# Performance work log

Measured on AMD Instinct MI355X. Metric: run time of the kernel, lower is better.

The kernel has to match this reference:

```python
import jax, jax.numpy as jnp
import numpy as np

B, T, DIM, H, DH, DT = 2, 2048, 1024, 16, 64, 32
Q_TEMP, K_TEMP = 1.0, 1.0
EPS = float(np.finfo(np.float32).eps)  # torch RMSNorm default eps for fp32
INV_SQRT_DH = 1.0 / np.sqrt(DH)


def _get_time(length, head_time_delta, time_angles, with_time_delta):
    # [T,1,1] positions, optionally offset per head -> [T,H,1]
    pos = jnp.arange(length, dtype=jnp.float32)[:, None, None]
    if with_time_delta:
        pos = pos + head_time_delta[None, :, None]          # [T,H,1]
    else:
        pos = jnp.broadcast_to(pos, (length, H, 1))          # [T,H,1]
    ang = pos * time_angles                                  # [T,H,Dt]
    c, s = jnp.cos(ang), jnp.sin(ang)
    return jnp.concatenate([c + s, c - s], axis=-1) * INV_SQRT_DH  # [T,H,2Dt]


def setup_inputs() -> dict:
    key = jax.random.key(0)
    ks = jax.random.split(key, 6)
    sc = 0.02
    states = jax.random.normal(ks[0], (B, T, DIM), jnp.float32)
    attention_mask = jnp.ones((B, T), jnp.int32)
    ln_w = jnp.ones((DIM,), jnp.float32)
    time_angles = 10000.0 ** (-1.0 / jnp.arange(1, DT + 1, dtype=jnp.float32))
    head_time_delta = jax.random.uniform(ks[1], (H,), jnp.float32)
    Wq = jax.random.normal(ks[2], (H * DH, DIM), jnp.float32) * sc
    q_bias = jnp.zeros((H * DH,), jnp.float32)
    Wk = jax.random.normal(ks[3], (H * DH, DIM), jnp.float32) * sc
    bk = jnp.zeros((H * DH,), jnp.float32)
    Wv = jax.random.normal(ks[4], (H * DH, DIM), jnp.float32) * sc
    bv = jnp.zeros((H * DH,), jnp.float32)
    Wo = jax.random.normal(ks[5], (DIM, H * DH), jnp.float32) * sc
    bo = jnp.zeros((DIM,), jnp.float32)
    return dict(states=states, attention_mask=attention_mask, ln_w=ln_w,
                time_angles=time_angles, head_time_delta=head_time_delta,
                Wq=Wq, q_bias=q_bias, Wk=Wk, bk=bk, Wv=Wv, bv=bv, Wo=Wo, bo=bo)


def reference(states, attention_mask, ln_w, time_angles, head_time_delta,
              Wq, q_bias, Wk, bk, Wv, bv, Wo, bo):
    # RMSNorm
    x = states * jax.lax.rsqrt(jnp.mean(states * states, axis=-1, keepdims=True) + EPS) * ln_w
    m = attention_mask.astype(x.dtype)[:, :, None, None]   # [B,T,1,1]

    # Q path -> q_attentioned [B,T,T,H]
    q = (x @ Wq.T - jnp.exp(q_bias)).reshape(B, T, H, DH)
    q_sm = jax.nn.softmax(q / Q_TEMP * m, axis=-1)
    t_q = _get_time(T, head_time_delta, time_angles, True)   # [T,H,2Dt]
    t_k = _get_time(T, head_time_delta, time_angles, False)  # [T,H,2Dt]
    q_timed = jnp.sum(q_sm, axis=-1, keepdims=True) * t_q    # [B,T,H,2Dt]
    q_att = jnp.einsum('bthd,lhd->btlh', q_timed, t_k)       # [B,T,T,H]

    # KV path
    k = (x @ Wk.T + bk).reshape(B, T, H, DH)
    k_sm = jax.nn.softmax(k / K_TEMP * m, axis=-1)
    v = (x @ Wv.T + bv).reshape(B, T, H, DH)
    kv = k_sm * v                                            # [B,T,H,Dh]

    loading = jnp.einsum('btlh,blhd->bthd', q_att, kv)       # [B,T,H,Dh]
    return loading.reshape(B, T, DIM) @ Wo.T + bo
```

## Files before the change

kernel.cpp:

```cpp
#include <hip/hip_runtime.h>
#include <math.h>

#define T_ 2048
#define H_ 16

typedef __attribute__((ext_vector_type(8))) short bfx8;
typedef __attribute__((ext_vector_type(4))) float f32x4;

__device__ __forceinline__ short f2bf(float f) {
  union { float f; unsigned u; } x; x.f = f;
  unsigned r = (x.u + 0x7FFFu + ((x.u >> 16) & 1u)) >> 16;
  return (short)r;
}
__device__ __forceinline__ float bf2f(short s) {
  union { unsigned u; float f; } x;
  x.u = ((unsigned)(unsigned short)s) << 16;
  return x.f;
}

#define GLD_LDS(g, l) \
  __builtin_amdgcn_global_load_lds( \
      (const __attribute__((address_space(1))) void*)(g), \
      (__attribute__((address_space(3))) void*)(l), 16, 0, 0)

__global__ __launch_bounds__(256) void prep_kernel(
    const float* __restrict__ Wk, const float* __restrict__ Wv,
    const float* __restrict__ Wo, const float* __restrict__ angles,
    const float* __restrict__ states, const float* __restrict__ ln_w,
    short* __restrict__ Wkb, short* __restrict__ Wvb, short* __restrict__ Wob,
    short* __restrict__ xb, short* __restrict__ Cb, short* __restrict__ tkT,
    float* __restrict__ MtH) {
  const int blk = blockIdx.x;
  if (blk < 3072) {
    const int i = blk * 256 + threadIdx.x;
    const int which = i >> 18;
    const int idx = i & 262143;
    const float* s = (which == 0) ? Wk : (which == 1) ? Wv : Wo;
    short* d = (which == 0) ? Wkb : (which == 1) ? Wvb : Wob;
    const float4 v = ((const float4*)s)[idx];
    short4 r;
    r.x = f2bf(v.x); r.y = f2bf(v.y); r.z = f2bf(v.z); r.w = f2bf(v.w);
    ((short4*)d)[idx] = r;
  } else if (blk < 7168) {
    const int row = blk - 3072;
    const int tid = threadIdx.x;
    const float4 v = ((const float4*)(states + (size_t)row * 1024))[tid];
    float ss = v.x * v.x + v.y * v.y + v.z * v.z + v.w * v.w;
#pragma unroll
    for (int off = 32; off >= 1; off >>= 1) ss += __shfl_xor(ss, off);
    __shared__ float red[4];
    if ((tid & 63) == 0) red[tid >> 6] = ss;
    __syncthreads();
    const float tot = red[0] + red[1] + red[2] + red[3];
    const float scale = rsqrtf(tot * (1.0f / 1024.0f) + 1.1920928955078125e-07f);
    const float4 w = ((const float4*)ln_w)[tid];
    short4 o;
    o.x = f2bf(v.x * scale * w.x);
    o.y = f2bf(v.y * scale * w.y);
    o.z = f2bf(v.z * scale * w.z);
    o.w = f2bf(v.w * scale * w.w);
    ((short4*)(xb + (size_t)row * 1024))[tid] = o;
  } else if (blk < 7424) {
    const int gid = (blk - 7168) * 256 + threadIdx.x;
    const int j = gid & 31;
    const int t = gid >> 5;
    float s, c;
    sincosf((float)t * angles[j], &s, &c);
    Cb[(size_t)t * 64 + j] = f2bf(0.125f * c);
    Cb[(size_t)t * 64 + 32 + j] = f2bf(0.125f * s);
  } else if (blk < 7456) {
    const int gid = (blk - 7424) * 256 + threadIdx.x;
    const int tc = gid & 255;
    const int j = gid >> 8;
    const float th = angles[j];
    short lo[8], hi[8];
#pragma unroll
    for (int r = 0; r < 8; ++r) {
      float s, c;
      sincosf((float)(tc * 8 + r) * th, &s, &c);
      lo[r] = f2bf((c + s) * 0.125f);
      hi[r] = f2bf((c - s) * 0.125f);
    }
    short* base = tkT + (size_t)j * 2048 + tc * 8;
    *(short4*)(base) = *(short4*)&lo[0];
    *(short4*)(base + 4) = *(short4*)&lo[4];
    short* base2 = tkT + (size_t)(32 + j) * 2048 + tc * 8;
    *(short4*)(base2) = *(short4*)&hi[0];
    *(short4*)(base2 + 4) = *(short4*)&hi[4];
  } else {
    const int gid = (blk - 7456) * 256 + threadIdx.x;
    ((float4*)MtH)[gid] = make_float4(0.f, 0.f, 0.f, 0.f);
  }
}

__global__ __launch_bounds__(256) void kvgemm_kernel(
    const short* __restrict__ xb, const short* __restrict__ Wkb,
    const short* __restrict__ Wvb, const float* __restrict__ bk,
    const float* __restrict__ bv, const int* __restrict__ mask,
    const short* __restrict__ tkT, float* __restrict__ Mt) {
  __shared__ short smem[16384];
  __shared__ short Vs[128][64];
  short(*As)[64] = (short(*)[64])smem;
  short(*Bk)[64] = (short(*)[64])(smem + 8192);
  short(*Bv)[64] = (short(*)[64])(smem + 12288);
  short(*kvS)[132] = (short(*)[132])smem;

  const int row0 = blockIdx.x * 128;
  const int h = blockIdx.y;
  const int t = threadIdx.x;
  const int lane = t & 63;
  const int wv = t >> 6;
  const bool isV = wv >= 2;
  const int wrow = (wv & 1) * 64;
  const int lrow = lane & 15;

  const int srow8 = t >> 3;
  const int kslotS = (t & 7) ^ (srow8 & 7);
  const short* gaS = xb + (size_t)(row0 + srow8) * 1024 + kslotS * 8;
  const short* gkS = Wkb + (size_t)(h * 64 + srow8) * 1024 + kslotS * 8;
  const short* gvS = Wvb + (size_t)(h * 64 + srow8) * 1024 + kslotS * 8;
  short* laS = &As[srow8][(t & 7) * 8];
  short* lkS = &Bk[srow8][(t & 7) * 8];
  short* lvS = &Bv[srow8][(t & 7) * 8];

  f32x4 acc[4][4] = {};
  for (int k0 = 0; k0 < 1024; k0 += 64) {
    GLD_LDS(gaS + k0, laS);
    GLD_LDS(gaS + 32 * 1024 + k0, laS + 2048);
    GLD_LDS(gaS + 64 * 1024 + k0, laS + 4096);
    GLD_LDS(gaS + 96 * 1024 + k0, laS + 6144);
    GLD_LDS(gkS + k0, lkS);
    GLD_LDS(gkS + 32 * 1024 + k0, lkS + 2048);
    GLD_LDS(gvS + k0, lvS);
    GLD_LDS(gvS + 32 * 1024 + k0, lvS + 2048);
    __syncthreads();
#pragma unroll
    for (int kk = 0; kk < 2; ++kk) {
      const int pcol = ((kk * 4 + (lane >> 4)) ^ (lrow & 7)) * 8;
      bfx8 af[4], bf_[4];
#pragma unroll
      for (int i = 0; i < 4; ++i)
        af[i] = *(const bfx8*)&As[wrow + i * 16 + lrow][pcol];
      const short(*Bs)[64] = isV ? Bv : Bk;
#pragma unroll
      for (int j = 0; j < 4; ++j)
        bf_[j] = *(const bfx8*)&Bs[j * 16 + lrow][pcol];
#pragma unroll
      for (int i = 0; i < 4; ++i)
#pragma unroll
        for (int j = 0; j < 4; ++j)
          acc[i][j] = __builtin_amdgcn_mfma_f32_16x16x32_bf16(af[i], bf_[j], acc[i][j], 0, 0, 0);
    }
    __syncthreads();
  }
  const int rq = (lane >> 4) * 4;
  if (isV) {
#pragma unroll
    for (int j = 0; j < 4; ++j) {
      const float bb = bv[h * 64 + j * 16 + lrow];
#pragma unroll
      for (int i = 0; i < 4; ++i)
#pragma unroll
        for (int rr = 0; rr < 4; ++rr)
          Vs[wrow + rq + i * 16 + rr][j * 16 + lrow] = f2bf(acc[i][j][rr] + bb);
    }
  }
  __syncthreads();
  if (!isV) {
    float bkc[4];
#pragma unroll
    for (int j = 0; j < 4; ++j) bkc[j] = bk[h * 64 + j * 16 + lrow];
    const int rowg0 = row0 + wrow + rq;
#pragma unroll
    for (int i = 0; i < 4; ++i) {
#pragma unroll
      for (int rr = 0; rr < 4; ++rr) {
        const float m = (float)mask[rowg0 + i * 16 + rr];
        float kf[4];
#pragma unroll
        for (int j = 0; j < 4; ++j) kf[j] = (acc[i][j][rr] + bkc[j]) * m;
        float mx = fmaxf(fmaxf(kf[0], kf[1]), fmaxf(kf[2], kf[3]));
#pragma unroll
        for (int off = 8; off >= 1; off >>= 1) mx = fmaxf(mx, __shfl_xor(mx, off));
        float s = 0.0f;
#pragma unroll
        for (int j = 0; j < 4; ++j) { kf[j] = expf(kf[j] - mx); s += kf[j]; }
#pragma unroll
        for (int off = 8; off >= 1; off >>= 1) s += __shfl_xor(s, off);
        const float inv = 1.0f / s;
#pragma unroll
        for (int j = 0; j < 4; ++j)
          acc[i][j][rr] = kf[j] * inv *
                          bf2f(Vs[wrow + rq + i * 16 + rr][j * 16 + lrow]);
      }
    }
#pragma unroll
    for (int j = 0; j < 4; ++j) {
      const int d = j * 16 + lrow;
#pragma unroll
      for (int i = 0; i < 4; ++i) {
        short4 o;
        o.x = f2bf(acc[i][j][0]); o.y = f2bf(acc[i][j][1]);
        o.z = f2bf(acc[i][j][2]); o.w = f2bf(acc[i][j][3]);
        *(short4*)&kvS[d][wrow + rq + i * 16] = o;
      }
    }
  }
  __syncthreads();
  const int bb = row0 >> 11;
  const int tb = row0 & 2047;
  const short* tkb = tkT + (size_t)(wv * 16 + lrow) * 2048 + tb;
  const int kg = (lane >> 4) * 8;
  f32x4 macc[4] = {};
#pragma unroll
  for (int kc = 0; kc < 4; ++kc) {
    const bfx8 af = *(const bfx8*)(tkb + kc * 32 + kg);
#pragma unroll
    for (int j = 0; j < 4; ++j) {
      const bfx8 bf_ = *(const bfx8*)&kvS[j * 16 + lrow][kc * 32 + kg];
      macc[j] = __builtin_amdgcn_mfma_f32_16x16x32_bf16(af, bf_, macc[j], 0, 0, 0);
    }
  }
  float* Mb = Mt + (size_t)(bb * 16 + h) * 4096;
#pragma unroll
  for (int j = 0; j < 4; ++j) {
    const int d = j * 16 + lrow;
#pragma unroll
    for (int rr = 0; rr < 4; ++rr) {
      const int e = wv * 16 + rq + rr;
      atomicAdd(&Mb[(size_t)e * 64 + d], macc[j][rr]);
    }
  }
}

__global__ __launch_bounds__(256) void foldhgemm_kernel(
    const short* __restrict__ Wob, const float* __restrict__ Mt,
    const float* __restrict__ angles, const float* __restrict__ delta,
    float* __restrict__ H) {
  const int bid = blockIdx.x;
  const int t = threadIdx.x;
  const int lane = t & 63;
  const int w = t >> 6;
  const int lrow = lane & 15;
  const int kg = (lane >> 4) * 8;
  const int h2 = bid & 7;
  const int ot = (bid >> 3) & 15;
  const int b = bid >> 7;
  const int orow = ot * 64 + w * 16 + lrow;
  float p[2][2], q[2][2];
#pragma unroll
  for (int hh = 0; hh < 2; ++hh) {
    const float dl = delta[h2 * 2 + hh];
#pragma unroll
    for (int aa = 0; aa < 2; ++aa) {
      float s, c;
      sincosf(dl * angles[aa * 16 + lrow], &s, &c);
      p[hh][aa] = c + s;
      q[hh][aa] = c - s;
    }
  }
  f32x4 acc[4] = {};
#pragma unroll
  for (int ks = 0; ks < 4; ++ks) {
    const int hh = ks >> 1;
    const int h = h2 * 2 + hh;
    const int d0 = (ks & 1) * 32 + kg;
    const float* Mthb = Mt + (size_t)(b * 16 + h) * 4096;
    const bfx8 af = *(const bfx8*)(Wob + (size_t)orow * 1024 + h * 64 + d0);
    float m0a[8], m1a[8], m0b[8], m1b[8];
    *(float4*)&m0a[0] = *(const float4*)(Mthb + lrow * 64 + d0);
    *(float4*)&m0a[4] = *(const float4*)(Mthb + lrow * 64 + d0 + 4);
    *(float4*)&m1a[0] = *(const float4*)(Mthb + (32 + lrow) * 64 + d0);
    *(float4*)&m1a[4] = *(const float4*)(Mthb + (32 + lrow) * 64 + d0 + 4);
    *(float4*)&m0b[0] = *(const float4*)(Mthb + (16 + lrow) * 64 + d0);
    *(float4*)&m0b[4] = *(const float4*)(Mthb + (16 + lrow) * 64 + d0 + 4);
    *(float4*)&m1b[0] = *(const float4*)(Mthb + (48 + lrow) * 64 + d0);
    *(float4*)&m1b[4] = *(const float4*)(Mthb + (48 + lrow) * 64 + d0 + 4);
    bfx8 bf0, bf1, bf2, bf3;
#pragma unroll
    for (int e = 0; e < 8; ++e) {
      bf0[e] = f2bf(p[hh][0] * m0a[e] + q[hh][0] * m1a[e]);
      bf1[e] = f2bf(p[hh][1] * m0b[e] + q[hh][1] * m1b[e]);
      bf2[e] = f2bf(q[hh][0] * m0a[e] - p[hh][0] * m1a[e]);
      bf3[e] = f2bf(q[hh][1] * m0b[e] - p[hh][1] * m1b[e]);
    }
    acc[0] = __builtin_amdgcn_mfma_f32_16x16x32_bf16(af, bf0, acc[0], 0, 0, 0);
    acc[1] = __builtin_amdgcn_mfma_f32_16x16x32_bf16(af, bf1, acc[1], 0, 0, 0);
    acc[2] = __builtin_amdgcn_mfma_f32_16x16x32_bf16(af, bf2, acc[2], 0, 0, 0);
    acc[3] = __builtin_amdgcn_mfma_f32_16x16x32_bf16(af, bf3, acc[3], 0, 0, 0);
  }
  float* Hb = H + (size_t)b * 65536;
  const int rq = (lane >> 4) * 4;
#pragma unroll
  for (int j = 0; j < 4; ++j) {
    const int kap = j * 16 + lrow;
#pragma unroll
    for (int rr = 0; rr < 4; ++rr) {
      const int o = ot * 64 + w * 16 + rq + rr;
      atomicAdd(&Hb[(size_t)o * 64 + kap], acc[j][rr]);
    }
  }
}

__global__ __launch_bounds__(256) void ofinal_kernel(
    const short* __restrict__ Cb, const float* __restrict__ H,
    const float* __restrict__ bo, float* __restrict__ out) {
  const int col0 = blockIdx.x * 128;
  const int row0 = blockIdx.y * 128;
  const int b = blockIdx.z;
  float* C = out + (size_t)b * 2097152;
  const float* Hb = H + (size_t)b * 65536;
  const int t = threadIdx.x;
  const int lane = t & 63;
  const int wv = t >> 6;
  const int wm = (wv & 1) * 64, wn = (wv >> 1) * 64;
  const int lrow = lane & 15;
  const int kg = (lane >> 4) * 8;
  f32x4 acc[4][4] = {};
#pragma unroll
  for (int k0 = 0; k0 < 64; k0 += 32) {
    bfx8 af[4], bf_[4];
#pragma unroll
    for (int i = 0; i < 4; ++i)
      af[i] = *(const bfx8*)(Cb + (size_t)(row0 + wm + i * 16 + lrow) * 64 + k0 + kg);
#pragma unroll
    for (int j = 0; j < 4; ++j) {
      const float* hp = Hb + (size_t)(col0 + wn + j * 16 + lrow) * 64 + k0 + kg;
      const float4 h0 = *(const float4*)hp;
      const float4 h1 = *(const float4*)(hp + 4);
      bfx8 bb;
      bb[0] = f2bf(h0.x); bb[1] = f2bf(h0.y); bb[2] = f2bf(h0.z); bb[3] = f2bf(h0.w);
      bb[4] = f2bf(h1.x); bb[5] = f2bf(h1.y); bb[6] = f2bf(h1.z); bb[7] = f2bf(h1.w);
      bf_[j] = bb;
    }
#pragma unroll
    for (int i = 0; i < 4; ++i)
#pragma unroll
      for (int j = 0; j < 4; ++j)
        acc[i][j] = __builtin_amdgcn_mfma_f32_16x16x32_bf16(af[i], bf_[j], acc[i][j], 0, 0, 0);
  }
  const int rq = (lane >> 4) * 4;
#pragma unroll
  for (int j = 0; j < 4; ++j) {
    const int c = col0 + wn + j * 16 + lrow;
    const float bb = bo[c];
#pragma unroll
    for (int i = 0; i < 4; ++i) {
      const int r = row0 + wm + i * 16 + rq;
#pragma unroll
      for (int rr = 0; rr < 4; ++rr)
        C[(size_t)(r + rr) * 1024 + c] = acc[i][j][rr] + bb;
    }
  }
}

extern "C" void kernel_launch(void* const* d_in, const int* in_sizes, int n_in,
                              void* d_out, int out_size, void* d_ws, size_t ws_size,
                              hipStream_t stream) {
  (void)in_sizes; (void)n_in; (void)out_size; (void)ws_size;
  const float* states = (const float*)d_in[0];
  const int* mask = (const int*)d_in[1];
  const float* ln_w = (const float*)d_in[2];
  const float* angles = (const float*)d_in[3];
  const float* delta = (const float*)d_in[4];
  const float* Wk = (const float*)d_in[7];
  const float* bk = (const float*)d_in[8];
  const float* Wv = (const float*)d_in[9];
  const float* bv = (const float*)d_in[10];
  const float* Wo = (const float*)d_in[11];
  const float* bo = (const float*)d_in[12];
  float* out = (float*)d_out;

  char* W = (char*)d_ws;
  short* xb  = (short*)(W);
  short* Wkb = (short*)(W + (8u << 20));
  short* Wvb = (short*)(W + (10u << 20));
  short* Wob = (short*)(W + (12u << 20));
  short* Cb  = (short*)(W + (14u << 20));
  short* tkT = (short*)(W + (14u << 20) + (256u << 10));
  float* Mt  = (float*)(W + (15u << 20));
  float* H   = (float*)(W + (15u << 20) + (512u << 10));

  prep_kernel<<<7712, 256, 0, stream>>>(Wk, Wv, Wo, angles, states, ln_w,
                                        Wkb, Wvb, Wob, xb, Cb, tkT, Mt);
  kvgemm_kernel<<<dim3(32, 16), 256, 0, stream>>>(xb, Wkb, Wvb, bk, bv, mask,
                                                  tkT, Mt);
  foldhgemm_kernel<<<256, 256, 0, stream>>>(Wob, Mt, angles, delta, H);
  ofinal_kernel<<<dim3(8, 16, 2), 256, 0, stream>>>(Cb, H, bo, out);
}
```

Baseline: 148.4 us.

## Double K-step per barrier and remap kvgemm blocks for XCD locality

The K/V GEMM now loads two 64-wide K slices per iteration into a doubled shared-memory buffer, which halves the number of __syncthreads barriers and gives more loads in flight per step. The 2D grid is flattened to 1D and block IDs are remapped so that blocks on the same XCD (id&7) share row blocks and heads, improving L2 reuse of x and the weights. The cost is twice the LDS per block, which can lower occupancy.

```diff
diff --git a/kernel.cpp b/kernel.cpp
--- a/kernel.cpp
+++ b/kernel.cpp
@@ -98,15 +98,17 @@
     const short* __restrict__ Wvb, const float* __restrict__ bk,
     const float* __restrict__ bv, const int* __restrict__ mask,
     const short* __restrict__ tkT, float* __restrict__ Mt) {
-  __shared__ short smem[16384];
+  __shared__ short smem[32768];
   __shared__ short Vs[128][64];
-  short(*As)[64] = (short(*)[64])smem;
-  short(*Bk)[64] = (short(*)[64])(smem + 8192);
-  short(*Bv)[64] = (short(*)[64])(smem + 12288);
   short(*kvS)[132] = (short(*)[132])smem;
 
-  const int row0 = blockIdx.x * 128;
-  const int h = blockIdx.y;
+  const int id = blockIdx.x;
+  const int wxcd = id & 7;
+  const int wi = id >> 3;
+  const int rb = ((wxcd >> 1) << 3) | (wi >> 3);
+  const int h = ((wxcd & 1) << 3) | (wi & 7);
+  const int row0 = rb * 128;
+
   const int t = threadIdx.x;
   const int lane = t & 63;
   const int wv = t >> 6;
@@ -119,12 +121,12 @@
   const short* gaS = xb + (size_t)(row0 + srow8) * 1024 + kslotS * 8;
   const short* gkS = Wkb + (size_t)(h * 64 + srow8) * 1024 + kslotS * 8;
   const short* gvS = Wvb + (size_t)(h * 64 + srow8) * 1024 + kslotS * 8;
-  short* laS = &As[srow8][(t & 7) * 8];
-  short* lkS = &Bk[srow8][(t & 7) * 8];
-  short* lvS = &Bv[srow8][(t & 7) * 8];
+  short* laS = smem + srow8 * 64 + (t & 7) * 8;
+  short* lkS = smem + 8192 + srow8 * 64 + (t & 7) * 8;
+  short* lvS = smem + 12288 + srow8 * 64 + (t & 7) * 8;
 
   f32x4 acc[4][4] = {};
-  for (int k0 = 0; k0 < 1024; k0 += 64) {
+  for (int k0 = 0; k0 < 1024; k0 += 128) {
     GLD_LDS(gaS + k0, laS);
     GLD_LDS(gaS + 32 * 1024 + k0, laS + 2048);
     GLD_LDS(gaS + 64 * 1024 + k0, laS + 4096);
@@ -133,23 +135,37 @@
     GLD_LDS(gkS + 32 * 1024 + k0, lkS + 2048);
     GLD_LDS(gvS + k0, lvS);
     GLD_LDS(gvS + 32 * 1024 + k0, lvS + 2048);
+    GLD_LDS(gaS + k0 + 64, laS + 16384);
+    GLD_LDS(gaS + 32 * 1024 + k0 + 64, laS + 16384 + 2048);
+    GLD_LDS(gaS + 64 * 1024 + k0 + 64, laS + 16384 + 4096);
+    GLD_LDS(gaS + 96 * 1024 + k0 + 64, laS + 16384 + 6144);
+    GLD_LDS(gkS + k0 + 64, lkS + 16384);
+    GLD_LDS(gkS + 32 * 1024 + k0 + 64, lkS + 16384 + 2048);
+    GLD_LDS(gvS + k0 + 64, lvS + 16384);
+    GLD_LDS(gvS + 32 * 1024 + k0 + 64, lvS + 16384 + 2048);
     __syncthreads();
 #pragma unroll
-    for (int kk = 0; kk < 2; ++kk) {
-      const int pcol = ((kk * 4 + (lane >> 4)) ^ (lrow & 7)) * 8;
-      bfx8 af[4], bf_[4];
-#pragma unroll
-      for (int i = 0; i < 4; ++i)
-        af[i] = *(const bfx8*)&As[wrow + i * 16 + lrow][pcol];
-      const short(*Bs)[64] = isV ? Bv : Bk;
-#pragma unroll
-      for (int j = 0; j < 4; ++j)
-        bf_[j] = *(const bfx8*)&Bs[j * 16 + lrow][pcol];
-#pragma unroll
-      for (int i = 0; i < 4; ++i)
+    for (int s = 0; s < 2; ++s) {
+      const short(*As)[64] = (const short(*)[64])(smem + s * 16384);
+      const short(*Bk)[64] = (const short(*)[64])(smem + s * 16384 + 8192);
+      const short(*Bv)[64] = (const short(*)[64])(smem + s * 16384 + 12288);
+#pragma unroll
+      for (int kk = 0; kk < 2; ++kk) {
+        const int pcol = ((kk * 4 + (lane >> 4)) ^ (lrow & 7)) * 8;
+        bfx8 af[4], bf_[4];
+#pragma unroll
+        for (int i = 0; i < 4; ++i)
+          af[i] = *(const bfx8*)&As[wrow + i * 16 + lrow][pcol];
+        const short(*Bs)[64] = isV ? Bv : Bk;
 #pragma unroll
         for (int j = 0; j < 4; ++j)
-          acc[i][j] = __builtin_amdgcn_mfma_f32_16x16x32_bf16(af[i], bf_[j], acc[i][j], 0, 0, 0);
+          bf_[j] = *(const bfx8*)&Bs[j * 16 + lrow][pcol];
+#pragma unroll
+        for (int i = 0; i < 4; ++i)
+#pragma unroll
+          for (int j = 0; j < 4; ++j)
+            acc[i][j] = __builtin_amdgcn_mfma_f32_16x16x32_bf16(af[i], bf_[j], acc[i][j], 0, 0, 0);
+      }
     }
     __syncthreads();
   }
@@ -383,8 +399,7 @@
 
   prep_kernel<<<7712, 256, 0, stream>>>(Wk, Wv, Wo, angles, states, ln_w,
                                         Wkb, Wvb, Wob, xb, Cb, tkT, Mt);
-  kvgemm_kernel<<<dim3(32, 16), 256, 0, stream>>>(xb, Wkb, Wvb, bk, bv, mask,
-                                                  tkT, Mt);
+  kvgemm_kernel<<<512, 256, 0, stream>>>(xb, Wkb, Wvb, bk, bv, mask, tkT, Mt);
   foldhgemm_kernel<<<256, 256, 0, stream>>>(Wob, Mt, angles, delta, H);
   ofinal_kernel<<<dim3(8, 16, 2), 256, 0, stream>>>(Cb, H, bo, out);
 }
```

Result: slower. 166.0 us (+11.8%).

## Load GEMM operands directly from global memory into registers, dropping LDS staging

Applied to the files above, without the earlier changes.

The K/V projection GEMM used to stage x and weight tiles in shared memory with async global-to-LDS loads and barriers. Each wave now reads its MFMA fragments straight from global memory into registers, with no shared staging and no per-iteration barriers. This removes LDS traffic and synchronisation. In exchange, data that waves could share is now fetched redundantly through L1/L2, the 8-element row reads are less coalesced, and nothing is prefetched to hide memory latency.

```diff
diff --git a/kernel.cpp b/kernel.cpp
--- a/kernel.cpp
+++ b/kernel.cpp
@@ -17,11 +17,6 @@
   x.u = ((unsigned)(unsigned short)s) << 16;
   return x.f;
 }
-
-#define GLD_LDS(g, l) \
-  __builtin_amdgcn_global_load_lds( \
-      (const __attribute__((address_space(1))) void*)(g), \
-      (__attribute__((address_space(3))) void*)(l), 16, 0, 0)
 
 __global__ __launch_bounds__(256) void prep_kernel(
     const float* __restrict__ Wk, const float* __restrict__ Wv,
@@ -98,12 +93,8 @@
     const short* __restrict__ Wvb, const float* __restrict__ bk,
     const float* __restrict__ bv, const int* __restrict__ mask,
     const short* __restrict__ tkT, float* __restrict__ Mt) {
-  __shared__ short smem[16384];
   __shared__ short Vs[128][64];
-  short(*As)[64] = (short(*)[64])smem;
-  short(*Bk)[64] = (short(*)[64])(smem + 8192);
-  short(*Bv)[64] = (short(*)[64])(smem + 12288);
-  short(*kvS)[132] = (short(*)[132])smem;
+  __shared__ short kvS[64][132];
 
   const int row0 = blockIdx.x * 128;
   const int h = blockIdx.y;
@@ -113,56 +104,42 @@
   const bool isV = wv >= 2;
   const int wrow = (wv & 1) * 64;
   const int lrow = lane & 15;
-
-  const int srow8 = t >> 3;
-  const int kslotS = (t & 7) ^ (srow8 & 7);
-  const short* gaS = xb + (size_t)(row0 + srow8) * 1024 + kslotS * 8;
-  const short* gkS = Wkb + (size_t)(h * 64 + srow8) * 1024 + kslotS * 8;
-  const short* gvS = Wvb + (size_t)(h * 64 + srow8) * 1024 + kslotS * 8;
-  short* laS = &As[srow8][(t & 7) * 8];
-  short* lkS = &Bk[srow8][(t & 7) * 8];
-  short* lvS = &Bv[srow8][(t & 7) * 8];
+  const int kgg = (lane >> 4) * 8;
+
+  const short* WB = isV ? Wvb : Wkb;
+  const short* ab[4];
+  const short* bb[4];
+#pragma unroll
+  for (int i = 0; i < 4; ++i)
+    ab[i] = xb + (size_t)(row0 + wrow + i * 16 + lrow) * 1024 + kgg;
+#pragma unroll
+  for (int j = 0; j < 4; ++j)
+    bb[j] = WB + (size_t)(h * 64 + j * 16 + lrow) * 1024 + kgg;
 
   f32x4 acc[4][4] = {};
-  for (int k0 = 0; k0 < 1024; k0 += 64) {
-    GLD_LDS(gaS + k0, laS);
-    GLD_LDS(gaS + 32 * 1024 + k0, laS + 2048);
-    GLD_LDS(gaS + 64 * 1024 + k0, laS + 4096);
-    GLD_LDS(gaS + 96 * 1024 + k0, laS + 6144);
-    GLD_LDS(gkS + k0, lkS);
-    GLD_LDS(gkS + 32 * 1024 + k0, lkS + 2048);
-    GLD_LDS(gvS + k0, lvS);
-    GLD_LDS(gvS + 32 * 1024 + k0, lvS + 2048);
-    __syncthreads();
-#pragma unroll
-    for (int kk = 0; kk < 2; ++kk) {
-      const int pcol = ((kk * 4 + (lane >> 4)) ^ (lrow & 7)) * 8;
-      bfx8 af[4], bf_[4];
-#pragma unroll
-      for (int i = 0; i < 4; ++i)
-        af[i] = *(const bfx8*)&As[wrow + i * 16 + lrow][pcol];
-      const short(*Bs)[64] = isV ? Bv : Bk;
+  for (int kc = 0; kc < 32; ++kc) {
+    bfx8 af[4], bf_[4];
+#pragma unroll
+    for (int i = 0; i < 4; ++i) af[i] = *(const bfx8*)(ab[i] + kc * 32);
+#pragma unroll
+    for (int j = 0; j < 4; ++j) bf_[j] = *(const bfx8*)(bb[j] + kc * 32);
+#pragma unroll
+    for (int i = 0; i < 4; ++i)
 #pragma unroll
       for (int j = 0; j < 4; ++j)
-        bf_[j] = *(const bfx8*)&Bs[j * 16 + lrow][pcol];
-#pragma unroll
-      for (int i = 0; i < 4; ++i)
-#pragma unroll
-        for (int j = 0; j < 4; ++j)
-          acc[i][j] = __builtin_amdgcn_mfma_f32_16x16x32_bf16(af[i], bf_[j], acc[i][j], 0, 0, 0);
-    }
-    __syncthreads();
-  }
+        acc[i][j] = __builtin_amdgcn_mfma_f32_16x16x32_bf16(af[i], bf_[j], acc[i][j], 0, 0, 0);
+  }
+
   const int rq = (lane >> 4) * 4;
   if (isV) {
 #pragma unroll
     for (int j = 0; j < 4; ++j) {
-      const float bb = bv[h * 64 + j * 16 + lrow];
+      const float bb2 = bv[h * 64 + j * 16 + lrow];
 #pragma unroll
       for (int i = 0; i < 4; ++i)
 #pragma unroll
         for (int rr = 0; rr < 4; ++rr)
-          Vs[wrow + rq + i * 16 + rr][j * 16 + lrow] = f2bf(acc[i][j][rr] + bb);
+          Vs[wrow + rq + i * 16 + rr][j * 16 + lrow] = f2bf(acc[i][j][rr] + bb2);
     }
   }
   __syncthreads();
@@ -207,7 +184,7 @@
     }
   }
   __syncthreads();
-  const int bb = row0 >> 11;
+  const int bbb = row0 >> 11;
   const int tb = row0 & 2047;
   const short* tkb = tkT + (size_t)(wv * 16 + lrow) * 2048 + tb;
   const int kg = (lane >> 4) * 8;
@@ -221,7 +198,7 @@
       macc[j] = __builtin_amdgcn_mfma_f32_16x16x32_bf16(af, bf_, macc[j], 0, 0, 0);
     }
   }
-  float* Mb = Mt + (size_t)(bb * 16 + h) * 4096;
+  float* Mb = Mt + (size_t)(bbb * 16 + h) * 4096;
 #pragma unroll
   for (int j = 0; j < 4; ++j) {
     const int d = j * 16 + lrow;
```

New measurement: 185.1 us. 24.7% more time.

## Replace atomic accumulations with partial buffers reduced in consumer kernels

Applied to the files above, without the earlier changes.

The kvgemm and foldhgemm kernels now write per-block partial results to separate slices instead of doing float atomicAdd into shared Mt and H. The consumer kernels (foldhgemm, ofinal) sum the 16 or 8 partials when they load, with foldhgemm staging the reduced Mt in shared memory. This removes atomic contention and the zero-init blocks in prep_kernel. In exchange it uses more workspace and adds redundant partial-sum reads in every consumer block.

```diff
diff --git a/kernel.cpp b/kernel.cpp
--- a/kernel.cpp
+++ b/kernel.cpp
@@ -28,8 +28,7 @@
     const float* __restrict__ Wo, const float* __restrict__ angles,
     const float* __restrict__ states, const float* __restrict__ ln_w,
     short* __restrict__ Wkb, short* __restrict__ Wvb, short* __restrict__ Wob,
-    short* __restrict__ xb, short* __restrict__ Cb, short* __restrict__ tkT,
-    float* __restrict__ MtH) {
+    short* __restrict__ xb, short* __restrict__ Cb, short* __restrict__ tkT) {
   const int blk = blockIdx.x;
   if (blk < 3072) {
     const int i = blk * 256 + threadIdx.x;
@@ -68,7 +67,7 @@
     sincosf((float)t * angles[j], &s, &c);
     Cb[(size_t)t * 64 + j] = f2bf(0.125f * c);
     Cb[(size_t)t * 64 + 32 + j] = f2bf(0.125f * s);
-  } else if (blk < 7456) {
+  } else {
     const int gid = (blk - 7424) * 256 + threadIdx.x;
     const int tc = gid & 255;
     const int j = gid >> 8;
@@ -87,9 +86,6 @@
     short* base2 = tkT + (size_t)(32 + j) * 2048 + tc * 8;
     *(short4*)(base2) = *(short4*)&hi[0];
     *(short4*)(base2 + 4) = *(short4*)&hi[4];
-  } else {
-    const int gid = (blk - 7456) * 256 + threadIdx.x;
-    ((float4*)MtH)[gid] = make_float4(0.f, 0.f, 0.f, 0.f);
   }
 }
 
@@ -97,7 +93,7 @@
     const short* __restrict__ xb, const short* __restrict__ Wkb,
     const short* __restrict__ Wvb, const float* __restrict__ bk,
     const float* __restrict__ bv, const int* __restrict__ mask,
-    const short* __restrict__ tkT, float* __restrict__ Mt) {
+    const short* __restrict__ tkT, float* __restrict__ Mtp) {
   __shared__ short smem[16384];
   __shared__ short Vs[128][64];
   short(*As)[64] = (short(*)[64])smem;
@@ -207,7 +203,8 @@
     }
   }
   __syncthreads();
-  const int bb = row0 >> 11;
+  const int bb = blockIdx.x >> 4;
+  const int rbl = blockIdx.x & 15;
   const int tb = row0 & 2047;
   const short* tkb = tkT + (size_t)(wv * 16 + lrow) * 2048 + tb;
   const int kg = (lane >> 4) * 8;
@@ -221,22 +218,23 @@
       macc[j] = __builtin_amdgcn_mfma_f32_16x16x32_bf16(af, bf_, macc[j], 0, 0, 0);
     }
   }
-  float* Mb = Mt + (size_t)(bb * 16 + h) * 4096;
+  float* Mb = Mtp + (((size_t)(bb * 16 + h) * 16) + rbl) * 4096;
 #pragma unroll
   for (int j = 0; j < 4; ++j) {
     const int d = j * 16 + lrow;
 #pragma unroll
     for (int rr = 0; rr < 4; ++rr) {
       const int e = wv * 16 + rq + rr;
-      atomicAdd(&Mb[(size_t)e * 64 + d], macc[j][rr]);
+      Mb[(size_t)e * 64 + d] = macc[j][rr];
     }
   }
 }
 
 __global__ __launch_bounds__(256) void foldhgemm_kernel(
-    const short* __restrict__ Wob, const float* __restrict__ Mt,
+    const short* __restrict__ Wob, const float* __restrict__ Mtp,
     const float* __restrict__ angles, const float* __restrict__ delta,
-    float* __restrict__ H) {
+    float* __restrict__ Hp) {
+  __shared__ float MtS[2][64][72];
   const int bid = blockIdx.x;
   const int t = threadIdx.x;
   const int lane = t & 63;
@@ -246,6 +244,24 @@
   const int h2 = bid & 7;
   const int ot = (bid >> 3) & 15;
   const int b = bid >> 7;
+
+  for (int f = t; f < 2048; f += 256) {
+    const int hh = f >> 10;
+    const int rem = f & 1023;
+    const int e = rem >> 4;
+    const int d4 = (rem & 15) * 4;
+    const float* src = Mtp + ((size_t)(b * 16 + h2 * 2 + hh) * 16) * 4096 +
+                       (size_t)e * 64 + d4;
+    float4 sum = *(const float4*)src;
+#pragma unroll
+    for (int rbl = 1; rbl < 16; ++rbl) {
+      const float4 v = *(const float4*)(src + (size_t)rbl * 4096);
+      sum.x += v.x; sum.y += v.y; sum.z += v.z; sum.w += v.w;
+    }
+    *(float4*)&MtS[hh][e][d4] = sum;
+  }
+  __syncthreads();
+
   const int orow = ot * 64 + w * 16 + lrow;
   float p[2][2], q[2][2];
 #pragma unroll
@@ -265,17 +281,16 @@
     const int hh = ks >> 1;
     const int h = h2 * 2 + hh;
     const int d0 = (ks & 1) * 32 + kg;
-    const float* Mthb = Mt + (size_t)(b * 16 + h) * 4096;
     const bfx8 af = *(const bfx8*)(Wob + (size_t)orow * 1024 + h * 64 + d0);
     float m0a[8], m1a[8], m0b[8], m1b[8];
-    *(float4*)&m0a[0] = *(const float4*)(Mthb + lrow * 64 + d0);
-    *(float4*)&m0a[4] = *(const float4*)(Mthb + lrow * 64 + d0 + 4);
-    *(float4*)&m1a[0] = *(const float4*)(Mthb + (32 + lrow) * 64 + d0);
-    *(float4*)&m1a[4] = *(const float4*)(Mthb + (32 + lrow) * 64 + d0 + 4);
-    *(float4*)&m0b[0] = *(const float4*)(Mthb + (16 + lrow) * 64 + d0);
-    *(float4*)&m0b[4] = *(const float4*)(Mthb + (16 + lrow) * 64 + d0 + 4);
-    *(float4*)&m1b[0] = *(const float4*)(Mthb + (48 + lrow) * 64 + d0);
-    *(float4*)&m1b[4] = *(const float4*)(Mthb + (48 + lrow) * 64 + d0 + 4);
+    *(float4*)&m0a[0] = *(const float4*)&MtS[hh][lrow][d0];
+    *(float4*)&m0a[4] = *(const float4*)&MtS[hh][lrow][d0 + 4];
+    *(float4*)&m1a[0] = *(const float4*)&MtS[hh][32 + lrow][d0];
+    *(float4*)&m1a[4] = *(const float4*)&MtS[hh][32 + lrow][d0 + 4];
+    *(float4*)&m0b[0] = *(const float4*)&MtS[hh][16 + lrow][d0];
+    *(float4*)&m0b[4] = *(const float4*)&MtS[hh][16 + lrow][d0 + 4];
+    *(float4*)&m1b[0] = *(const float4*)&MtS[hh][48 + lrow][d0];
+    *(float4*)&m1b[4] = *(const float4*)&MtS[hh][48 + lrow][d0 + 4];
     bfx8 bf0, bf1, bf2, bf3;
 #pragma unroll
     for (int e = 0; e < 8; ++e) {
@@ -289,7 +304,7 @@
     acc[2] = __builtin_amdgcn_mfma_f32_16x16x32_bf16(af, bf2, acc[2], 0, 0, 0);
     acc[3] = __builtin_amdgcn_mfma_f32_16x16x32_bf16(af, bf3, acc[3], 0, 0, 0);
   }
-  float* Hb = H + (size_t)b * 65536;
+  float* Hb = Hp + (size_t)(h2 * 2 + b) * 65536;
   const int rq = (lane >> 4) * 4;
 #pragma unroll
   for (int j = 0; j < 4; ++j) {
@@ -297,19 +312,18 @@
 #pragma unroll
     for (int rr = 0; rr < 4; ++rr) {
       const int o = ot * 64 + w * 16 + rq + rr;
-      atomicAdd(&Hb[(size_t)o * 64 + kap], acc[j][rr]);
+      Hb[(size_t)o * 64 + kap] = acc[j][rr];
     }
   }
 }
 
 __global__ __launch_bounds__(256) void ofinal_kernel(
-    const short* __restrict__ Cb, const float* __restrict__ H,
+    const short* __restrict__ Cb, const float* __restrict__ Hp,
     const float* __restrict__ bo, float* __restrict__ out) {
   const int col0 = blockIdx.x * 128;
   const int row0 = blockIdx.y * 128;
   const int b = blockIdx.z;
   float* C = out + (size_t)b * 2097152;
-  const float* Hb = H + (size_t)b * 65536;
   const int t = threadIdx.x;
   const int lane = t & 63;
   const int wv = t >> 6;
@@ -325,9 +339,17 @@
       af[i] = *(const bfx8*)(Cb + (size_t)(row0 + wm + i * 16 + lrow) * 64 + k0 + kg);
 #pragma unroll
     for (int j = 0; j < 4; ++j) {
-      const float* hp = Hb + (size_t)(col0 + wn + j * 16 + lrow) * 64 + k0 + kg;
-      const float4 h0 = *(const float4*)hp;
-      const float4 h1 = *(const float4*)(hp + 4);
+      const size_t off = (size_t)(col0 + wn + j * 16 + lrow) * 64 + k0 + kg;
+      float4 h0 = make_float4(0.f, 0.f, 0.f, 0.f);
+      float4 h1 = make_float4(0.f, 0.f, 0.f, 0.f);
+#pragma unroll
+      for (int s = 0; s < 8; ++s) {
+        const float* P = Hp + (size_t)(s * 2 + b) * 65536 + off;
+        const float4 a0 = *(const float4*)P;
+        const float4 a1 = *(const float4*)(P + 4);
+        h0.x += a0.x; h0.y += a0.y; h0.z += a0.z; h0.w += a0.w;
+        h1.x += a1.x; h1.y += a1.y; h1.z += a1.z; h1.w += a1.w;
+      }
       bfx8 bb;
       bb[0] = f2bf(h0.x); bb[1] = f2bf(h0.y); bb[2] = f2bf(h0.z); bb[3] = f2bf(h0.w);
       bb[4] = f2bf(h1.x); bb[5] = f2bf(h1.y); bb[6] = f2bf(h1.z); bb[7] = f2bf(h1.w);
@@ -378,13 +400,13 @@
   short* Wob = (short*)(W + (12u << 20));
   short* Cb  = (short*)(W + (14u << 20));
   short* tkT = (short*)(W + (14u << 20) + (256u << 10));
-  float* Mt  = (float*)(W + (15u << 20));
-  float* H   = (float*)(W + (15u << 20) + (512u << 10));
-
-  prep_kernel<<<7712, 256, 0, stream>>>(Wk, Wv, Wo, angles, states, ln_w,
-                                        Wkb, Wvb, Wob, xb, Cb, tkT, Mt);
+  float* Mtp = (float*)(W + (15u << 20));
+  float* Hp  = (float*)(W + (23u << 20));
+
+  prep_kernel<<<7456, 256, 0, stream>>>(Wk, Wv, Wo, angles, states, ln_w,
+                                        Wkb, Wvb, Wob, xb, Cb, tkT);
   kvgemm_kernel<<<dim3(32, 16), 256, 0, stream>>>(xb, Wkb, Wvb, bk, bv, mask,
-                                                  tkT, Mt);
-  foldhgemm_kernel<<<256, 256, 0, stream>>>(Wob, Mt, angles, delta, H);
-  ofinal_kernel<<<dim3(8, 16, 2), 256, 0, stream>>>(Cb, H, bo, out);
-}
+                                                  tkT, Mtp);
+  foldhgemm_kernel<<<256, 256, 0, stream>>>(Wob, Mtp, angles, delta, Hp);
+  ofinal_kernel<<<dim3(8, 16, 2), 256, 0, stream>>>(Cb, Hp, bo, out);
+}
```

Result: slower. 158.2 us (+6.6%).
